# Performance work log

Measured on AMD Instinct MI355X. Metric: run time of the kernel, lower is better.

## Reference

```python
import jax, jax.numpy as jnp
import numpy as np

DIM, HEADS, NB_FEATURES = 512, 8, 64
HEAD_DIM = DIM // HEADS


def setup_inputs() -> dict:
    key = jax.random.key(0)
    k_x, k_qkv, k_pm, k_wp, k_bp = jax.random.split(key, 5)
    B, N = 8, 4096
    x = jax.random.normal(k_x, (B, N, DIM), dtype=jnp.float32)
    # to_qkv: Linear(dim, 3*dim, bias=False) -> apply as x @ w_qkv
    w_qkv = jax.random.normal(k_qkv, (DIM, 3 * DIM), dtype=jnp.float32) * (1.0 / np.sqrt(DIM))
    # random projection buffer [H, D, F]
    proj_mat = jax.random.normal(k_pm, (HEADS, HEAD_DIM, NB_FEATURES), dtype=jnp.float32)
    # output projection Linear(dim, dim) with bias
    w_proj = jax.random.normal(k_wp, (DIM, DIM), dtype=jnp.float32) * (1.0 / np.sqrt(DIM))
    b_proj = jax.random.normal(k_bp, (DIM,), dtype=jnp.float32) * 0.01
    return {"x": x, "w_qkv": w_qkv, "proj_mat": proj_mat, "w_proj": w_proj, "b_proj": b_proj}


def _phi(t, proj_mat):
    # t: [B,N,H,D], proj_mat: [H,D,F] -> [B,N,H,F]
    return jax.nn.elu(jnp.einsum('bnhd,hdf->bnhf', t, proj_mat)) + 1.0


def reference(x, w_qkv, proj_mat, w_proj, b_proj):
    B, N, dim = x.shape
    H, D = HEADS, dim // HEADS
    qkv = x @ w_qkv  # [B,N,3*dim]
    q, k, v = jnp.split(qkv, 3, axis=-1)
    q = q.reshape(B, N, H, D)
    k = k.reshape(B, N, H, D)
    v = v.reshape(B, N, H, D)
    q_phi = _phi(q, proj_mat)  # [B,N,H,F]
    k_phi = _phi(k, proj_mat)  # [B,N,H,F]
    kv = jnp.einsum('bnhf,bnhd->bhfd', k_phi, v)  # [B,H,F,D]
    z = 1.0 / jnp.einsum('bnhf,bhf->bnh', q_phi, k_phi.sum(axis=1))  # [B,N,H]
    out = jnp.einsum('bnhf,bhfd,bnh->bnhd', q_phi, kv, z)  # [B,N,H,D]
    out = out.reshape(B, N, H * D)
    return out @ w_proj + b_proj
```

## Files before the change

### kernel.cpp

```cpp
#include <hip/hip_runtime.h>
#include <hip/hip_bf16.h>

typedef __bf16 bf16_t;
typedef __bf16 bf16x4 __attribute__((ext_vector_type(4)));
typedef __bf16 bf16x8 __attribute__((ext_vector_type(8)));
typedef float f32x4 __attribute__((ext_vector_type(4)));

__device__ __forceinline__ void gload16(const void* g, void* l) {
  __builtin_amdgcn_global_load_lds((const __attribute__((address_space(1))) void*)g,
                                   (__attribute__((address_space(3))) void*)l, 16, 0, 0);
}

__global__ __launch_bounds__(256) void prep_qk(const float* __restrict__ w_qkv,
                                               const float* __restrict__ proj,
                                               bf16_t* __restrict__ WeffT) {
  const int half = blockIdx.x >> 3, h = blockIdx.x & 7;
  const int i0 = blockIdx.y * 64;
  __shared__ float P[64 * 64];
  __shared__ float Wt[64][65];
  const int t = threadIdx.x;
  #pragma unroll
  for (int r = 0; r < 16; ++r) P[t + 256 * r] = proj[(size_t)h * 4096 + t + 256 * r];
  #pragma unroll
  for (int r = 0; r < 16; ++r) {
    const int idx = t + 256 * r;
    Wt[idx >> 6][idx & 63] =
        w_qkv[(size_t)(i0 + (idx >> 6)) * 1536 + half * 512 + h * 64 + (idx & 63)];
  }
  __syncthreads();
  const int i = t & 63, fg = t >> 6;
  for (int f = fg; f < 64; f += 4) {
    float s = 0.f;
    #pragma unroll
    for (int d = 0; d < 64; ++d) s += Wt[i][d] * P[d * 64 + f];
    WeffT[(size_t)(half * 512 + h * 64 + f) * 512 + i0 + i] = (bf16_t)s;
  }
}

__global__ __launch_bounds__(256) void prep_v(const float* __restrict__ w_qkv,
                                              bf16_t* __restrict__ WeffT) {
  __shared__ bf16_t tile[32][33];
  const int i0 = blockIdx.x * 32, n0 = blockIdx.y * 32;
  const int tn = threadIdx.x & 31, ti = threadIdx.x >> 5;
  #pragma unroll
  for (int p = 0; p < 4; ++p) {
    const int i = ti + p * 8;
    tile[i][tn] = (bf16_t)w_qkv[(size_t)(i0 + i) * 1536 + 1024 + n0 + tn];
  }
  __syncthreads();
  #pragma unroll
  for (int p = 0; p < 4; ++p) {
    const int n = ti + p * 8;
    WeffT[(size_t)(1024 + n0 + n) * 512 + i0 + tn] = tile[tn][n];
  }
}

__global__ __launch_bounds__(256) void cast_x(const f32x4* __restrict__ x,
                                              bf16x4* __restrict__ xb, int n4) {
  int i = blockIdx.x * 256 + threadIdx.x;
  if (i < n4) {
    f32x4 v = x[i];
    bf16x4 o;
    #pragma unroll
    for (int j = 0; j < 4; ++j) o[j] = (bf16_t)v[j];
    xb[i] = o;
  }
}

__global__ __launch_bounds__(256) void gemm_qkv(const bf16_t* __restrict__ x_bf,
                                                const bf16_t* __restrict__ WeffT,
                                                bf16_t* __restrict__ q_phi,
                                                bf16_t* __restrict__ kT,
                                                bf16_t* __restrict__ vT) {
  constexpr int K = 512, BK = 64;
  __shared__ alignas(16) char smem[65536];
  const int t = threadIdx.x, w = t >> 6, l = t & 63;
  const int hw = blockIdx.x;
  const int bid = (hw & 7) * 384 + (hw >> 3);
  const int tok_blk = bid / 12, cb = bid % 12;
  const size_t tok0 = (size_t)tok_blk * 128;
  const bool qpath = (cb < 4);
  const bf16_t* Pp = qpath ? (WeffT + (size_t)cb * 128 * 512) : (x_bf + tok0 * 512);
  const bf16_t* Qp = qpath ? (x_bf + tok0 * 512)
                           : (WeffT + (size_t)(512 + (cb - 4) * 128) * 512);

  const int wr = w >> 1, wc = w & 1;
  const int lrow = l & 15, lkb = l >> 4;
  const int st_r = l >> 3;
  const int st_c = ((l & 7) ^ st_r) * 8;
  size_t p_src[4], q_src[4];
  #pragma unroll
  for (int c = 0; c < 4; ++c) {
    const int q8 = c * 4 + w;
    p_src[c] = (size_t)(q8 * 8 + st_r) * K + st_c;
    q_src[c] = (size_t)(q8 * 8 + st_r) * K + st_c;
  }

  f32x4 acc[4][4];
  #pragma unroll
  for (int m = 0; m < 4; ++m)
    #pragma unroll
    for (int n = 0; n < 4; ++n) acc[m][n] = f32x4{0.f, 0.f, 0.f, 0.f};

  #pragma unroll
  for (int c = 0; c < 4; ++c) {
    const int q8 = c * 4 + w;
    gload16(Pp + p_src[c], smem + q8 * 1024);
    gload16(Qp + q_src[c], smem + 16384 + q8 * 1024);
  }
  __syncthreads();

  int cur = 0;
  for (int kt = 0; kt < K; kt += BK) {
    if (kt + BK < K) {
      char* nb = smem + (cur ^ 1) * 32768;
      #pragma unroll
      for (int c = 0; c < 4; ++c) {
        const int q8 = c * 4 + w;
        gload16(Pp + p_src[c] + kt + BK, nb + q8 * 1024);
        gload16(Qp + q_src[c] + kt + BK, nb + 16384 + q8 * 1024);
      }
    }
    const char* PsB = smem + cur * 32768;
    const char* QsB = PsB + 16384;
    bf16x8 pf[4][2], qf[4][2];
    #pragma unroll
    for (int m = 0; m < 4; ++m) {
      const int r = wr * 64 + m * 16 + lrow;
      #pragma unroll
      for (int kk = 0; kk < 2; ++kk) {
        const int kb = lkb + kk * 4;
        pf[m][kk] = *(const bf16x8*)(PsB + r * 128 + (((kb ^ (r & 7)) & 7) << 4));
      }
    }
    #pragma unroll
    for (int n = 0; n < 4; ++n) {
      const int r = wc * 64 + n * 16 + lrow;
      #pragma unroll
      for (int kk = 0; kk < 2; ++kk) {
        const int kb = lkb + kk * 4;
        qf[n][kk] = *(const bf16x8*)(QsB + r * 128 + (((kb ^ (r & 7)) & 7) << 4));
      }
    }
    #pragma unroll
    for (int m = 0; m < 4; ++m)
      #pragma unroll
      for (int n = 0; n < 4; ++n) {
        acc[m][n] = __builtin_amdgcn_mfma_f32_16x16x32_bf16(pf[m][0], qf[n][0], acc[m][n], 0, 0, 0);
        acc[m][n] = __builtin_amdgcn_mfma_f32_16x16x32_bf16(pf[m][1], qf[n][1], acc[m][n], 0, 0, 0);
      }
    __syncthreads();
    cur ^= 1;
  }

  bf16_t* ep = (bf16_t*)smem;
  const bool doElu = qpath || (cb < 8);
  #pragma unroll
  for (int n = 0; n < 4; ++n) {
    const int qc = wc * 64 + n * 16 + lrow;
    #pragma unroll
    for (int m = 0; m < 4; ++m) {
      const int pr0 = wr * 64 + m * 16 + lkb * 4;
      bf16x4 o;
      #pragma unroll
      for (int j = 0; j < 4; ++j) {
        float v = acc[m][n][j];
        if (doElu) v = v > 0.f ? v + 1.f : __expf(v);
        o[j] = (bf16_t)v;
      }
      const int u = pr0 >> 3;
      *(bf16x4*)((char*)ep + qc * 256 + ((u ^ (qc & 15)) << 4) + (pr0 & 7) * 2) = o;
    }
  }
  __syncthreads();
  #pragma unroll
  for (int i = 0; i < 8; ++i) {
    const int flat = i * 256 + t;
    const int qc2 = flat >> 4, u2 = flat & 15;
    bf16x8 vv = *(const bf16x8*)((char*)ep + qc2 * 256 + ((u2 ^ (qc2 & 15)) << 4));
    if (qpath) {
      *(bf16x8*)&q_phi[(tok0 + qc2) * 512 + cb * 128 + u2 * 8] = vv;
    } else {
      const int f512 = (cb - 4) * 128 + qc2;
      bf16_t* dst = (f512 < 512 ? kT + ((size_t)(tok0 >> 12) * 512 + f512) * 4096
                                : vT + ((size_t)(tok0 >> 12) * 512 + (f512 - 512)) * 4096) +
                    (tok0 & 4095) + u2 * 8;
      *(bf16x8*)dst = vv;
    }
  }
}

__global__ __launch_bounds__(256) void kv_mfma(const bf16_t* __restrict__ kT,
                                               const bf16_t* __restrict__ vT,
                                               float* __restrict__ kv,
                                               float* __restrict__ ksum) {
  const int bh = blockIdx.x;
  const int nbase = blockIdx.y * 512;
  __shared__ alignas(16) char smem[32768];
  const int t = threadIdx.x, w = t >> 6, l = t & 63;
  const int wr = w >> 1, wc = w & 1;
  const int lrow = l & 15, lkb = l >> 4;
  const int st_r = l >> 3;
  const int st_c = ((l & 7) ^ st_r) * 8;
  const bf16_t* Kp = kT + (size_t)bh * 64 * 4096;
  const bf16_t* Vp = vT + (size_t)bh * 64 * 4096;

  f32x4 acc[2][2];
  #pragma unroll
  for (int m = 0; m < 2; ++m)
    #pragma unroll
    for (int n = 0; n < 2; ++n) acc[m][n] = f32x4{0.f, 0.f, 0.f, 0.f};
  float ksf[2] = {0.f, 0.f};

  #pragma unroll
  for (int c = 0; c < 2; ++c) {
    const int q8 = w * 2 + c;
    gload16(Kp + (size_t)(q8 * 8 + st_r) * 4096 + nbase + st_c, smem + q8 * 1024);
    gload16(Vp + (size_t)(q8 * 8 + st_r) * 4096 + nbase + st_c, smem + 8192 + q8 * 1024);
  }
  __syncthreads();

  int cur = 0;
  for (int st = 0; st < 8; ++st) {
    if (st < 7) {
      char* nb = smem + (cur ^ 1) * 16384;
      const int nb2 = nbase + (st + 1) * 64;
      #pragma unroll
      for (int c = 0; c < 2; ++c) {
        const int q8 = w * 2 + c;
        gload16(Kp + (size_t)(q8 * 8 + st_r) * 4096 + nb2 + st_c, nb + q8 * 1024);
        gload16(Vp + (size_t)(q8 * 8 + st_r) * 4096 + nb2 + st_c, nb + 8192 + q8 * 1024);
      }
    }
    const char* KsB = smem + cur * 16384;
    const char* VsB = KsB + 8192;
    bf16x8 af[2][2], bf[2][2];
    #pragma unroll
    for (int m = 0; m < 2; ++m) {
      const int r = wr * 32 + m * 16 + lrow;
      #pragma unroll
      for (int kk = 0; kk < 2; ++kk) {
        const int kb = lkb + kk * 4;
        af[m][kk] = *(const bf16x8*)(KsB + r * 128 + (((kb ^ (r & 7)) & 7) << 4));
      }
    }
    #pragma unroll
    for (int n = 0; n < 2; ++n) {
      const int r = wc * 32 + n * 16 + lrow;
      #pragma unroll
      for (int kk = 0; kk < 2; ++kk) {
        const int kb = lkb + kk * 4;
        bf[n][kk] = *(const bf16x8*)(VsB + r * 128 + (((kb ^ (r & 7)) & 7) << 4));
      }
    }
    #pragma unroll
    for (int m = 0; m < 2; ++m)
      #pragma unroll
      for (int n = 0; n < 2; ++n) {
        acc[m][n] = __builtin_amdgcn_mfma_f32_16x16x32_bf16(af[m][0], bf[n][0], acc[m][n], 0, 0, 0);
        acc[m][n] = __builtin_amdgcn_mfma_f32_16x16x32_bf16(af[m][1], bf[n][1], acc[m][n], 0, 0, 0);
      }
    if (wc == 0) {
      #pragma unroll
      for (int m = 0; m < 2; ++m)
        #pragma unroll
        for (int kk = 0; kk < 2; ++kk)
          #pragma unroll
          for (int j = 0; j < 8; ++j) ksf[m] += (float)af[m][kk][j];
    }
    __syncthreads();
    cur ^= 1;
  }

  float* kvp = kv + (size_t)bh * 4096;
  #pragma unroll
  for (int m = 0; m < 2; ++m)
    #pragma unroll
    for (int n = 0; n < 2; ++n)
      #pragma unroll
      for (int j = 0; j < 4; ++j)
        atomicAdd(&kvp[(wr * 32 + m * 16 + lkb * 4 + j) * 64 + wc * 32 + n * 16 + lrow],
                  acc[m][n][j]);
  if (wc == 0) {
    #pragma unroll
    for (int m = 0; m < 2; ++m) {
      float s = ksf[m];
      s += __shfl_xor(s, 16);
      s += __shfl_xor(s, 32);
      if (l < 16) atomicAdd(&ksum[(size_t)bh * 64 + wr * 32 + m * 16 + l], s);
    }
  }
}

__global__ __launch_bounds__(256) void w2_kernel(const float* __restrict__ kv,
                                                 const float* __restrict__ w_proj,
                                                 bf16_t* __restrict__ W2T) {
  const int bh = blockIdx.x, b = bh >> 3, h = bh & 7;
  const int j0 = blockIdx.y * 64;
  const int t = threadIdx.x;
  __shared__ float kvs[64][64];
  __shared__ float wps[64][64];
  const float* kvp = kv + (size_t)bh * 4096;
  #pragma unroll
  for (int i = 0; i < 16; ++i) ((float*)kvs)[t + 256 * i] = kvp[t + 256 * i];
  {
    const int d = t >> 2, c16 = (t & 3) * 16;
    const float* src = w_proj + (size_t)(h * 64 + d) * 512 + j0 + c16;
    #pragma unroll
    for (int j = 0; j < 16; ++j) wps[d][c16 + j] = src[j];
  }
  __syncthreads();
  const int fq = t >> 4, jq = t & 15;
  float acc[4][4] = {};
  for (int d = 0; d < 64; ++d) {
    float kf[4], wj[4];
    #pragma unroll
    for (int i = 0; i < 4; ++i) kf[i] = kvs[fq * 4 + i][d];
    #pragma unroll
    for (int i = 0; i < 4; ++i) wj[i] = wps[d][jq * 4 + i];
    #pragma unroll
    for (int i = 0; i < 4; ++i)
      #pragma unroll
      for (int j = 0; j < 4; ++j) acc[i][j] += kf[i] * wj[j];
  }
  #pragma unroll
  for (int j = 0; j < 4; ++j)
    #pragma unroll
    for (int i = 0; i < 4; ++i)
      W2T[((size_t)b * 512 + j0 + jq * 4 + j) * 512 + h * 64 + fq * 4 + i] = (bf16_t)acc[i][j];
}

__global__ __launch_bounds__(256) void zq_kernel(const bf16_t* __restrict__ qphi,
                                                 const float* __restrict__ ksum,
                                                 bf16_t* __restrict__ zq) {
  const int row = blockIdx.x * 4 + (threadIdx.x >> 6);
  const int l = threadIdx.x & 63;
  const int b = row >> 12;
  const int h = l >> 3, f8 = (l & 7) * 8;
  const bf16_t* src = qphi + (size_t)row * 512 + h * 64 + f8;
  bf16x8 v = *(const bf16x8*)src;
  const float* ks = ksum + ((size_t)b * 8 + h) * 64 + f8;
  float part = 0.f;
  float vf[8];
  #pragma unroll
  for (int j = 0; j < 8; ++j) { vf[j] = (float)v[j]; part += vf[j] * ks[j]; }
  part += __shfl_xor(part, 1);
  part += __shfl_xor(part, 2);
  part += __shfl_xor(part, 4);
  const float z = 1.f / part;
  bf16x8 o;
  #pragma unroll
  for (int j = 0; j < 8; ++j) o[j] = (bf16_t)(vf[j] * z);
  *(bf16x8*)(zq + (size_t)row * 512 + h * 64 + f8) = o;
}

__global__ __launch_bounds__(256) void gemm_out(const bf16_t* __restrict__ W2T,
                                                const bf16_t* __restrict__ zq,
                                                float* __restrict__ Cout,
                                                const float* __restrict__ bias) {
  constexpr int K = 512, BK = 64;
  __shared__ alignas(16) char smem[65536];
  const int t = threadIdx.x, w = t >> 6, l = t & 63;
  const int hw = blockIdx.x;
  const int bid = (hw & 7) * 128 + (hw >> 3);
  const int z = bid >> 7;
  const int rem = bid & 127;
  const int qblk = rem >> 2, pblk = rem & 3;
  const size_t tok0 = (size_t)qblk * 128;
  const int pj0 = pblk * 128;
  const bf16_t* Pp = W2T + ((size_t)z * 512 + pj0) * 512;
  const bf16_t* Qp = zq + ((size_t)z * 4096 + tok0) * 512;

  const int wr = w >> 1, wc = w & 1;
  const int lrow = l & 15, lkb = l >> 4;
  const int st_r = l >> 3;
  const int st_c = ((l & 7) ^ st_r) * 8;

  f32x4 acc[4][4];
  #pragma unroll
  for (int m = 0; m < 4; ++m)
    #pragma unroll
    for (int n = 0; n < 4; ++n) acc[m][n] = f32x4{0.f, 0.f, 0.f, 0.f};

  #pragma unroll
  for (int c = 0; c < 4; ++c) {
    const int q8 = c * 4 + w;
    gload16(Pp + (size_t)(q8 * 8 + st_r) * K + st_c, smem + q8 * 1024);
    gload16(Qp + (size_t)(q8 * 8 + st_r) * K + st_c, smem + 16384 + q8 * 1024);
  }
  __syncthreads();

  int cur = 0;
  for (int kt = 0; kt < K; kt += BK) {
    if (kt + BK < K) {
      char* nb = smem + (cur ^ 1) * 32768;
      #pragma unroll
      for (int c = 0; c < 4; ++c) {
        const int q8 = c * 4 + w;
        gload16(Pp + (size_t)(q8 * 8 + st_r) * K + kt + BK + st_c, nb + q8 * 1024);
        gload16(Qp + (size_t)(q8 * 8 + st_r) * K + kt + BK + st_c, nb + 16384 + q8 * 1024);
      }
    }
    const char* PsB = smem + cur * 32768;
    const char* QsB = PsB + 16384;
    bf16x8 pf[4][2], qf[4][2];
    #pragma unroll
    for (int m = 0; m < 4; ++m) {
      const int r = wr * 64 + m * 16 + lrow;
      #pragma unroll
      for (int kk = 0; kk < 2; ++kk) {
        const int kb = lkb + kk * 4;
        pf[m][kk] = *(const bf16x8*)(PsB + r * 128 + (((kb ^ (r & 7)) & 7) << 4));
      }
    }
    #pragma unroll
    for (int n = 0; n < 4; ++n) {
      const int r = wc * 64 + n * 16 + lrow;
      #pragma unroll
      for (int kk = 0; kk < 2; ++kk) {
        const int kb = lkb + kk * 4;
        qf[n][kk] = *(const bf16x8*)(QsB + r * 128 + (((kb ^ (r & 7)) & 7) << 4));
      }
    }
    #pragma unroll
    for (int m = 0; m < 4; ++m)
      #pragma unroll
      for (int n = 0; n < 4; ++n) {
        acc[m][n] = __builtin_amdgcn_mfma_f32_16x16x32_bf16(pf[m][0], qf[n][0], acc[m][n], 0, 0, 0);
        acc[m][n] = __builtin_amdgcn_mfma_f32_16x16x32_bf16(pf[m][1], qf[n][1], acc[m][n], 0, 0, 0);
      }
    __syncthreads();
    cur ^= 1;
  }

  float* ep = (float*)smem;
  #pragma unroll
  for (int p = 0; p < 2; ++p) {
    if (p) __syncthreads();
    #pragma unroll
    for (int nn2 = 0; nn2 < 2; ++nn2) {
      const int n = p * 2 + nn2;
      const int r6 = wc * 32 + (n & 1) * 16 + lrow;
      #pragma unroll
      for (int m = 0; m < 4; ++m) {
        const int pr0 = wr * 64 + m * 16 + lkb * 4;
        f32x4 v = acc[m][n];
        const f32x4 bv = *(const f32x4*)&bias[pj0 + pr0];
        #pragma unroll
        for (int j = 0; j < 4; ++j) v[j] += bv[j];
        const int u = pr0 >> 2;
        *(f32x4*)((char*)ep + r6 * 512 + ((u ^ (r6 & 31)) << 4)) = v;
      }
    }
    __syncthreads();
    #pragma unroll
    for (int i = 0; i < 8; ++i) {
      const int flat = i * 256 + t;
      const int r6 = flat >> 5, u2 = flat & 31;
      f32x4 v = *(const f32x4*)((char*)ep + r6 * 512 + ((u2 ^ (r6 & 31)) << 4));
      const int qc = (r6 >> 5) * 64 + p * 32 + (r6 & 31);
      *(f32x4*)&Cout[((size_t)z * 4096 + tok0 + qc) * 512 + pj0 + u2 * 4] = v;
    }
  }
}

extern "C" void kernel_launch(void* const* d_in, const int* in_sizes, int n_in,
                              void* d_out, int out_size, void* d_ws, size_t ws_size,
                              hipStream_t stream) {
  const float* x      = (const float*)d_in[0];
  const float* w_qkv  = (const float*)d_in[1];
  const float* proj   = (const float*)d_in[2];
  const float* w_proj = (const float*)d_in[3];
  const float* b_proj = (const float*)d_in[4];
  float* out = (float*)d_out;
  char* ws = (char*)d_ws;

  bf16_t* x_bf  = (bf16_t*)(ws + 0);
  bf16_t* WeffT = (bf16_t*)(ws + 33554432);
  bf16_t* q_phi = (bf16_t*)(ws + 35127296);
  bf16_t* kT    = (bf16_t*)(ws + 68681728);
  bf16_t* vT    = (bf16_t*)(ws + 102236160);
  float*  kv    = (float*)(ws + 135790592);
  float*  ksum  = (float*)(ws + 136839168);
  bf16_t* W2T   = (bf16_t*)(ws + 136855552);
  bf16_t* zq    = (bf16_t*)(ws + 141049856);

  prep_qk<<<dim3(16, 8), 256, 0, stream>>>(w_qkv, proj, WeffT);
  prep_v<<<dim3(16, 16), 256, 0, stream>>>(w_qkv, WeffT);
  cast_x<<<16384, 256, 0, stream>>>((const f32x4*)x, (bf16x4*)x_bf, 4194304);
  gemm_qkv<<<3072, 256, 0, stream>>>(x_bf, WeffT, q_phi, kT, vT);
  hipMemsetAsync(kv, 0, 1048576 + 16384, stream);
  kv_mfma<<<dim3(64, 8), 256, 0, stream>>>(kT, vT, kv, ksum);
  w2_kernel<<<dim3(64, 8), 256, 0, stream>>>(kv, w_proj, W2T);
  zq_kernel<<<8192, 256, 0, stream>>>(q_phi, ksum, zq);
  gemm_out<<<1024, 256, 0, stream>>>(W2T, zq, out, b_proj);
}
```

Before: 184.2 us.

## Rewrite QKV GEMM with 256x256 tiles, 8 waves and 4-stage LDS pipeline

```diff
diff --git a/kernel.cpp b/kernel.cpp
--- a/kernel.cpp
+++ b/kernel.cpp
@@ -10,6 +10,9 @@
   __builtin_amdgcn_global_load_lds((const __attribute__((address_space(1))) void*)g,
                                    (__attribute__((address_space(3))) void*)l, 16, 0, 0);
 }
+
+#define SB() __builtin_amdgcn_sched_barrier(0)
+#define VMW(n) asm volatile("s_waitcnt vmcnt(" #n ")" ::: "memory")
 
 __global__ __launch_bounds__(256) void prep_qk(const float* __restrict__ w_qkv,
                                                const float* __restrict__ proj,
@@ -67,100 +70,105 @@
   }
 }
 
-__global__ __launch_bounds__(256) void gemm_qkv(const bf16_t* __restrict__ x_bf,
-                                                const bf16_t* __restrict__ WeffT,
-                                                bf16_t* __restrict__ q_phi,
-                                                bf16_t* __restrict__ kT,
-                                                bf16_t* __restrict__ vT) {
-  constexpr int K = 512, BK = 64;
-  __shared__ alignas(16) char smem[65536];
-  const int t = threadIdx.x, w = t >> 6, l = t & 63;
+__global__ __launch_bounds__(512, 2) void gemm_qkv8(const bf16_t* __restrict__ x_bf,
+                                                    const bf16_t* __restrict__ WeffT,
+                                                    bf16_t* __restrict__ q_phi,
+                                                    bf16_t* __restrict__ kT,
+                                                    bf16_t* __restrict__ vT) {
+  __shared__ alignas(16) char smem[131072];
+  const int t = threadIdx.x;
+  const int wid = t >> 6, l = t & 63;
+  const int wr = wid >> 2, wc = wid & 3;
+  const int lrow = l & 15, lkb = l >> 4;
   const int hw = blockIdx.x;
-  const int bid = (hw & 7) * 384 + (hw >> 3);
-  const int tok_blk = bid / 12, cb = bid % 12;
-  const size_t tok0 = (size_t)tok_blk * 128;
-  const bool qpath = (cb < 4);
-  const bf16_t* Pp = qpath ? (WeffT + (size_t)cb * 128 * 512) : (x_bf + tok0 * 512);
-  const bf16_t* Qp = qpath ? (x_bf + tok0 * 512)
-                           : (WeffT + (size_t)(512 + (cb - 4) * 128) * 512);
-
-  const int wr = w >> 1, wc = w & 1;
-  const int lrow = l & 15, lkb = l >> 4;
-  const int st_r = l >> 3;
-  const int st_c = ((l & 7) ^ st_r) * 8;
-  size_t p_src[4], q_src[4];
-  #pragma unroll
-  for (int c = 0; c < 4; ++c) {
-    const int q8 = c * 4 + w;
-    p_src[c] = (size_t)(q8 * 8 + st_r) * K + st_c;
-    q_src[c] = (size_t)(q8 * 8 + st_r) * K + st_c;
-  }
-
-  f32x4 acc[4][4];
-  #pragma unroll
-  for (int m = 0; m < 4; ++m)
+  const int bid = (hw & 7) * 96 + (hw >> 3);
+  const int tb = bid / 6, fb = bid % 6;
+  const size_t tok0 = (size_t)tb * 256;
+  const int f0 = fb * 256;
+  const bf16_t* Ap = x_bf + tok0 * 512;
+  const bf16_t* Bp = WeffT + (size_t)f0 * 512;
+
+  const int sr = t >> 2, su = t & 3;
+  const int f_sr = (sr >> 1) & 3;
+  const size_t a_off0 = (size_t)sr * 512 + ((su ^ f_sr) * 8);
+  const size_t a_off1 = (size_t)(sr + 128) * 512 + ((su ^ f_sr) * 8);
+
+  auto stageA = [&](int s) {
+    char* dst = smem + (s & 3) * 16384;
+    gload16(Ap + a_off0 + s * 32, dst + t * 16);
+    gload16(Ap + a_off1 + s * 32, dst + 8192 + t * 16);
+  };
+  auto stageB = [&](int s) {
+    char* dst = smem + 65536 + (s & 3) * 16384;
+    gload16(Bp + a_off0 + s * 32, dst + t * 16);
+    gload16(Bp + a_off1 + s * 32, dst + 8192 + t * 16);
+  };
+
+  int woff[8], xoff[4];
+  #pragma unroll
+  for (int m = 0; m < 8; ++m) {
+    const int r = wr * 128 + m * 16 + lrow;
+    woff[m] = r * 64 + ((lkb ^ ((r >> 1) & 3)) << 4);
+  }
+  #pragma unroll
+  for (int n = 0; n < 4; ++n) {
+    const int r = wc * 64 + n * 16 + lrow;
+    xoff[n] = r * 64 + ((lkb ^ ((r >> 1) & 3)) << 4);
+  }
+
+  f32x4 acc[8][4];
+  #pragma unroll
+  for (int m = 0; m < 8; ++m)
     #pragma unroll
     for (int n = 0; n < 4; ++n) acc[m][n] = f32x4{0.f, 0.f, 0.f, 0.f};
 
-  #pragma unroll
-  for (int c = 0; c < 4; ++c) {
-    const int q8 = c * 4 + w;
-    gload16(Pp + p_src[c], smem + q8 * 1024);
-    gload16(Qp + q_src[c], smem + 16384 + q8 * 1024);
-  }
-  __syncthreads();
-
-  int cur = 0;
-  for (int kt = 0; kt < K; kt += BK) {
-    if (kt + BK < K) {
-      char* nb = smem + (cur ^ 1) * 32768;
-      #pragma unroll
-      for (int c = 0; c < 4; ++c) {
-        const int q8 = c * 4 + w;
-        gload16(Pp + p_src[c] + kt + BK, nb + q8 * 1024);
-        gload16(Qp + q_src[c] + kt + BK, nb + 16384 + q8 * 1024);
-      }
-    }
-    const char* PsB = smem + cur * 32768;
-    const char* QsB = PsB + 16384;
-    bf16x8 pf[4][2], qf[4][2];
-    #pragma unroll
-    for (int m = 0; m < 4; ++m) {
-      const int r = wr * 64 + m * 16 + lrow;
-      #pragma unroll
-      for (int kk = 0; kk < 2; ++kk) {
-        const int kb = lkb + kk * 4;
-        pf[m][kk] = *(const bf16x8*)(PsB + r * 128 + (((kb ^ (r & 7)) & 7) << 4));
-      }
-    }
+  stageA(0); stageB(0); stageA(1); stageB(1); stageA(2); stageB(2);
+  VMW(8);
+  SB(); __builtin_amdgcn_s_barrier(); SB();
+
+  bf16x8 xf[4];
+  #pragma unroll
+  for (int kt = 0; kt < 16; ++kt) {
+    const char* Xs = smem + (kt & 3) * 16384;
+    const char* Ws = smem + 65536 + (kt & 3) * 16384;
+    bf16x8 wf[4];
+    #pragma unroll
+    for (int m = 0; m < 4; ++m) wf[m] = *(const bf16x8*)(Ws + woff[m]);
+    #pragma unroll
+    for (int n = 0; n < 4; ++n) xf[n] = *(const bf16x8*)(Xs + xoff[n]);
+    if (kt + 3 < 16) stageA(kt + 3);
+    SB(); __builtin_amdgcn_s_barrier(); SB();
+    __builtin_amdgcn_s_setprio(1);
+    #pragma unroll
+    for (int m = 0; m < 4; ++m)
+      #pragma unroll
+      for (int n = 0; n < 4; ++n)
+        acc[m][n] = __builtin_amdgcn_mfma_f32_16x16x32_bf16(wf[m], xf[n], acc[m][n], 0, 0, 0);
+    __builtin_amdgcn_s_setprio(0);
+    SB(); __builtin_amdgcn_s_barrier(); SB();
+    #pragma unroll
+    for (int m = 0; m < 4; ++m) wf[m] = *(const bf16x8*)(Ws + woff[4 + m]);
+    if (kt + 3 < 16) stageB(kt + 3);
+    if (kt <= 12) { VMW(8); } else if (kt == 13) { VMW(4); } else if (kt == 14) { VMW(0); }
+    SB(); __builtin_amdgcn_s_barrier(); SB();
+    __builtin_amdgcn_s_setprio(1);
+    #pragma unroll
+    for (int m = 0; m < 4; ++m)
+      #pragma unroll
+      for (int n = 0; n < 4; ++n)
+        acc[4 + m][n] = __builtin_amdgcn_mfma_f32_16x16x32_bf16(wf[m], xf[n], acc[4 + m][n], 0, 0, 0);
+    __builtin_amdgcn_s_setprio(0);
+    SB(); __builtin_amdgcn_s_barrier(); SB();
+  }
+
+  const bool doElu = (fb < 4);
+  #pragma unroll
+  for (int m = 0; m < 8; ++m) {
+    const int feat = wr * 128 + m * 16 + lkb * 4;
+    const int ub = feat >> 3, bo = (feat & 7) * 2;
     #pragma unroll
     for (int n = 0; n < 4; ++n) {
-      const int r = wc * 64 + n * 16 + lrow;
-      #pragma unroll
-      for (int kk = 0; kk < 2; ++kk) {
-        const int kb = lkb + kk * 4;
-        qf[n][kk] = *(const bf16x8*)(QsB + r * 128 + (((kb ^ (r & 7)) & 7) << 4));
-      }
-    }
-    #pragma unroll
-    for (int m = 0; m < 4; ++m)
-      #pragma unroll
-      for (int n = 0; n < 4; ++n) {
-        acc[m][n] = __builtin_amdgcn_mfma_f32_16x16x32_bf16(pf[m][0], qf[n][0], acc[m][n], 0, 0, 0);
-        acc[m][n] = __builtin_amdgcn_mfma_f32_16x16x32_bf16(pf[m][1], qf[n][1], acc[m][n], 0, 0, 0);
-      }
-    __syncthreads();
-    cur ^= 1;
-  }
-
-  bf16_t* ep = (bf16_t*)smem;
-  const bool doElu = qpath || (cb < 8);
-  #pragma unroll
-  for (int n = 0; n < 4; ++n) {
-    const int qc = wc * 64 + n * 16 + lrow;
-    #pragma unroll
-    for (int m = 0; m < 4; ++m) {
-      const int pr0 = wr * 64 + m * 16 + lkb * 4;
+      const int trow = wc * 64 + n * 16 + lrow;
       bf16x4 o;
       #pragma unroll
       for (int j = 0; j < 4; ++j) {
@@ -168,24 +176,38 @@
         if (doElu) v = v > 0.f ? v + 1.f : __expf(v);
         o[j] = (bf16_t)v;
       }
-      const int u = pr0 >> 3;
-      *(bf16x4*)((char*)ep + qc * 256 + ((u ^ (qc & 15)) << 4) + (pr0 & 7) * 2) = o;
+      const int s = (trow ^ (trow >> 3)) & 7;
+      *(bf16x4*)(smem + trow * 512 + ((ub ^ s) << 4) + bo) = o;
     }
   }
   __syncthreads();
-  #pragma unroll
-  for (int i = 0; i < 8; ++i) {
-    const int flat = i * 256 + t;
-    const int qc2 = flat >> 4, u2 = flat & 15;
-    bf16x8 vv = *(const bf16x8*)((char*)ep + qc2 * 256 + ((u2 ^ (qc2 & 15)) << 4));
-    if (qpath) {
-      *(bf16x8*)&q_phi[(tok0 + qc2) * 512 + cb * 128 + u2 * 8] = vv;
-    } else {
-      const int f512 = (cb - 4) * 128 + qc2;
-      bf16_t* dst = (f512 < 512 ? kT + ((size_t)(tok0 >> 12) * 512 + f512) * 4096
-                                : vT + ((size_t)(tok0 >> 12) * 512 + (f512 - 512)) * 4096) +
-                    (tok0 & 4095) + u2 * 8;
-      *(bf16x8*)dst = vv;
+  if (fb < 2) {
+    #pragma unroll
+    for (int p = 0; p < 16; ++p) {
+      const int flat = p * 512 + t;
+      const int trow = flat >> 5, u = flat & 31;
+      const int s = (trow ^ (trow >> 3)) & 7;
+      bf16x8 vv = *(const bf16x8*)(smem + trow * 512 + ((u ^ s) << 4));
+      *(bf16x8*)&q_phi[(tok0 + trow) * 512 + f0 + u * 8] = vv;
+    }
+  } else {
+    const int b = (int)(tok0 >> 12);
+    const int nn0 = (int)(tok0 & 4095);
+    bf16_t* base = (fb < 4) ? (kT + ((size_t)(b * 512 + (fb - 2) * 256)) * 4096)
+                            : (vT + ((size_t)(b * 512 + (fb - 4) * 256)) * 4096);
+    #pragma unroll
+    for (int p = 0; p < 16; ++p) {
+      const int fl = (p & 7) * 32 + (t >> 4);
+      const int tg = (p >> 3) * 16 + (t & 15);
+      const int ub = fl >> 3, bo = (fl & 7) * 2;
+      bf16x8 vv;
+      #pragma unroll
+      for (int j = 0; j < 8; ++j) {
+        const int tok = tg * 8 + j;
+        const int s = (tok ^ (tok >> 3)) & 7;
+        vv[j] = *(const bf16_t*)(smem + tok * 512 + ((ub ^ s) << 4) + bo);
+      }
+      *(bf16x8*)(base + (size_t)fl * 4096 + nn0 + tg * 8) = vv;
     }
   }
 }
@@ -488,7 +510,7 @@
   prep_qk<<<dim3(16, 8), 256, 0, stream>>>(w_qkv, proj, WeffT);
   prep_v<<<dim3(16, 16), 256, 0, stream>>>(w_qkv, WeffT);
   cast_x<<<16384, 256, 0, stream>>>((const f32x4*)x, (bf16x4*)x_bf, 4194304);
-  gemm_qkv<<<3072, 256, 0, stream>>>(x_bf, WeffT, q_phi, kT, vT);
+  gemm_qkv8<<<768, 512, 0, stream>>>(x_bf, WeffT, q_phi, kT, vT);
   hipMemsetAsync(kv, 0, 1048576 + 16384, stream);
   kv_mfma<<<dim3(64, 8), 256, 0, stream>>>(kT, vT, kv, ksum);
   w2_kernel<<<dim3(64, 8), 256, 0, stream>>>(kv, w_proj, W2T);
```

Result: no change. 185.9 us (+1.0%).

## Fuse z-normalisation of q_phi into output GEMM B-operand staging

Applied to the files above, without the earlier changes.

```diff
diff --git a/kernel.cpp b/kernel.cpp
--- a/kernel.cpp
+++ b/kernel.cpp
@@ -4,12 +4,15 @@
 typedef __bf16 bf16_t;
 typedef __bf16 bf16x4 __attribute__((ext_vector_type(4)));
 typedef __bf16 bf16x8 __attribute__((ext_vector_type(8)));
+typedef float f32x2 __attribute__((ext_vector_type(2)));
 typedef float f32x4 __attribute__((ext_vector_type(4)));
 
 __device__ __forceinline__ void gload16(const void* g, void* l) {
   __builtin_amdgcn_global_load_lds((const __attribute__((address_space(1))) void*)g,
                                    (__attribute__((address_space(3))) void*)l, 16, 0, 0);
 }
+
+#define VMW(n) asm volatile("s_waitcnt vmcnt(" #n ")" ::: "memory")
 
 __global__ __launch_bounds__(256) void prep_qk(const float* __restrict__ w_qkv,
                                                const float* __restrict__ proj,
@@ -330,36 +333,12 @@
       W2T[((size_t)b * 512 + j0 + jq * 4 + j) * 512 + h * 64 + fq * 4 + i] = (bf16_t)acc[i][j];
 }
 
-__global__ __launch_bounds__(256) void zq_kernel(const bf16_t* __restrict__ qphi,
-                                                 const float* __restrict__ ksum,
-                                                 bf16_t* __restrict__ zq) {
-  const int row = blockIdx.x * 4 + (threadIdx.x >> 6);
-  const int l = threadIdx.x & 63;
-  const int b = row >> 12;
-  const int h = l >> 3, f8 = (l & 7) * 8;
-  const bf16_t* src = qphi + (size_t)row * 512 + h * 64 + f8;
-  bf16x8 v = *(const bf16x8*)src;
-  const float* ks = ksum + ((size_t)b * 8 + h) * 64 + f8;
-  float part = 0.f;
-  float vf[8];
-  #pragma unroll
-  for (int j = 0; j < 8; ++j) { vf[j] = (float)v[j]; part += vf[j] * ks[j]; }
-  part += __shfl_xor(part, 1);
-  part += __shfl_xor(part, 2);
-  part += __shfl_xor(part, 4);
-  const float z = 1.f / part;
-  bf16x8 o;
-  #pragma unroll
-  for (int j = 0; j < 8; ++j) o[j] = (bf16_t)(vf[j] * z);
-  *(bf16x8*)(zq + (size_t)row * 512 + h * 64 + f8) = o;
-}
-
 __global__ __launch_bounds__(256) void gemm_out(const bf16_t* __restrict__ W2T,
-                                                const bf16_t* __restrict__ zq,
+                                                const bf16_t* __restrict__ q_phi,
+                                                const float* __restrict__ ksum,
                                                 float* __restrict__ Cout,
                                                 const float* __restrict__ bias) {
-  constexpr int K = 512, BK = 64;
-  __shared__ alignas(16) char smem[65536];
+  __shared__ alignas(16) char smem[67584];
   const int t = threadIdx.x, w = t >> 6, l = t & 63;
   const int hw = blockIdx.x;
   const int bid = (hw & 7) * 128 + (hw >> 3);
@@ -369,12 +348,67 @@
   const size_t tok0 = (size_t)qblk * 128;
   const int pj0 = pblk * 128;
   const bf16_t* Pp = W2T + ((size_t)z * 512 + pj0) * 512;
-  const bf16_t* Qp = zq + ((size_t)z * 4096 + tok0) * 512;
 
   const int wr = w >> 1, wc = w & 1;
   const int lrow = l & 15, lkb = l >> 4;
   const int st_r = l >> 3;
   const int st_c = ((l & 7) ^ st_r) * 8;
+  const int token = t >> 1, half = t & 1;
+  float* ks_lds = (float*)(smem + 65536);
+
+  bf16x8 breg[4];
+  auto loadB = [&](int c) {
+    const bf16_t* p = q_phi + ((size_t)z * 4096 + tok0 + token) * 512 + c * 64 + half * 32;
+    breg[0] = *(const bf16x8*)p;
+    breg[1] = *(const bf16x8*)(p + 8);
+    breg[2] = *(const bf16x8*)(p + 16);
+    breg[3] = *(const bf16x8*)(p + 24);
+  };
+  auto stageA = [&](int s) {
+    #pragma unroll
+    for (int c = 0; c < 4; ++c) {
+      const int q8 = c * 4 + w;
+      gload16(Pp + (size_t)(q8 * 8 + st_r) * 512 + s * 64 + st_c,
+              smem + (s & 1) * 16384 + q8 * 1024);
+    }
+  };
+  auto procB = [&](int c) {
+    const f32x4* ksv = (const f32x4*)(ks_lds + c * 64 + half * 32);
+    float vals[32];
+    float dot = 0.f;
+    #pragma unroll
+    for (int g = 0; g < 8; ++g) {
+      const f32x4 kk = ksv[g];
+      #pragma unroll
+      for (int j = 0; j < 4; ++j) {
+        const float v = (float)breg[g >> 1][(g & 1) * 4 + j];
+        vals[g * 4 + j] = v;
+        dot += v * kk[j];
+      }
+    }
+    dot += __shfl_xor(dot, 1);
+    const float zz = 1.f / dot;
+    char* dst = smem + 32768 + (c & 1) * 16384;
+    #pragma unroll
+    for (int g = 0; g < 4; ++g) {
+      bf16x8 o;
+      #pragma unroll
+      for (int j = 0; j < 8; ++j) o[j] = (bf16_t)(vals[g * 8 + j] * zz);
+      const int uk = half * 4 + g;
+      *(bf16x8*)(dst + token * 128 + ((uk ^ (token & 7)) << 4)) = o;
+    }
+  };
+
+  {
+    const f32x2 kk = *(const f32x2*)&ksum[(size_t)z * 512 + t * 2];
+    *(f32x2*)&ks_lds[t * 2] = kk;
+  }
+  __syncthreads();
+  loadB(0);
+  stageA(0);
+  procB(0);
+  VMW(0);
+  __syncthreads();
 
   f32x4 acc[4][4];
   #pragma unroll
@@ -382,27 +416,9 @@
     #pragma unroll
     for (int n = 0; n < 4; ++n) acc[m][n] = f32x4{0.f, 0.f, 0.f, 0.f};
 
-  #pragma unroll
-  for (int c = 0; c < 4; ++c) {
-    const int q8 = c * 4 + w;
-    gload16(Pp + (size_t)(q8 * 8 + st_r) * K + st_c, smem + q8 * 1024);
-    gload16(Qp + (size_t)(q8 * 8 + st_r) * K + st_c, smem + 16384 + q8 * 1024);
-  }
-  __syncthreads();
-
-  int cur = 0;
-  for (int kt = 0; kt < K; kt += BK) {
-    if (kt + BK < K) {
-      char* nb = smem + (cur ^ 1) * 32768;
-      #pragma unroll
-      for (int c = 0; c < 4; ++c) {
-        const int q8 = c * 4 + w;
-        gload16(Pp + (size_t)(q8 * 8 + st_r) * K + kt + BK + st_c, nb + q8 * 1024);
-        gload16(Qp + (size_t)(q8 * 8 + st_r) * K + kt + BK + st_c, nb + 16384 + q8 * 1024);
-      }
-    }
-    const char* PsB = smem + cur * 32768;
-    const char* QsB = PsB + 16384;
+  for (int kt = 0; kt < 8; ++kt) {
+    const char* PsB = smem + (kt & 1) * 16384;
+    const char* QsB = smem + 32768 + (kt & 1) * 16384;
     bf16x8 pf[4][2], qf[4][2];
     #pragma unroll
     for (int m = 0; m < 4; ++m) {
@@ -422,6 +438,7 @@
         qf[n][kk] = *(const bf16x8*)(QsB + r * 128 + (((kb ^ (r & 7)) & 7) << 4));
       }
     }
+    if (kt + 1 < 8) { loadB(kt + 1); stageA(kt + 1); }
     #pragma unroll
     for (int m = 0; m < 4; ++m)
       #pragma unroll
@@ -429,8 +446,8 @@
         acc[m][n] = __builtin_amdgcn_mfma_f32_16x16x32_bf16(pf[m][0], qf[n][0], acc[m][n], 0, 0, 0);
         acc[m][n] = __builtin_amdgcn_mfma_f32_16x16x32_bf16(pf[m][1], qf[n][1], acc[m][n], 0, 0, 0);
       }
+    if (kt + 1 < 8) { procB(kt + 1); VMW(0); }
     __syncthreads();
-    cur ^= 1;
   }
 
   float* ep = (float*)smem;
@@ -483,7 +500,6 @@
   float*  kv    = (float*)(ws + 135790592);
   float*  ksum  = (float*)(ws + 136839168);
   bf16_t* W2T   = (bf16_t*)(ws + 136855552);
-  bf16_t* zq    = (bf16_t*)(ws + 141049856);
 
   prep_qk<<<dim3(16, 8), 256, 0, stream>>>(w_qkv, proj, WeffT);
   prep_v<<<dim3(16, 16), 256, 0, stream>>>(w_qkv, WeffT);
@@ -492,6 +508,5 @@
   hipMemsetAsync(kv, 0, 1048576 + 16384, stream);
   kv_mfma<<<dim3(64, 8), 256, 0, stream>>>(kT, vT, kv, ksum);
   w2_kernel<<<dim3(64, 8), 256, 0, stream>>>(kv, w_proj, W2T);
-  zq_kernel<<<8192, 256, 0, stream>>>(q_phi, ksum, zq);
-  gemm_out<<<1024, 256, 0, stream>>>(W2T, zq, out, b_proj);
-}
+  gemm_out<<<1024, 256, 0, stream>>>(W2T, q_phi, ksum, out, b_proj);
+}
```

Result: faster. 175.2 us (-4.9%).
